# Performance work log

Hardware: AMD Instinct MI355X
Metric: run time of the kernel (lower is better)

Reference implementation:

```python
import jax, jax.numpy as jnp
import numpy as np

NUM_HEADS = 12
TOP_K = 4
LN_EPS = 1e-5


def _ln(x, w, b):
    m = jnp.mean(x, -1, keepdims=True)
    v = jnp.mean((x - m) ** 2, -1, keepdims=True)
    return (x - m) * jax.lax.rsqrt(v + LN_EPS) * w + b


def _attn(x, qkv_w, qkv_b, proj_w, proj_b):
    B, N, C = x.shape
    hd = C // NUM_HEADS
    qkv = (x @ qkv_w + qkv_b).reshape(B, N, 3, NUM_HEADS, hd)
    q, k, v = jnp.moveaxis(qkv, 2, 0)  # each [B,N,H,hd]
    attn = jax.nn.softmax(jnp.einsum('bnhd,bmhd->bhnm', q * hd ** -0.5, k), axis=-1)
    out = jnp.einsum('bhnm,bmhd->bnhd', attn, v).reshape(B, N, C)
    return out @ proj_w + proj_b


def _moe(x2, gate_w, w1, b1, w2, b2):
    # x2: [tokens, D]; vmoe-style token top-k gating (eval mode, no noise)
    Tt = x2.shape[0]
    E = gate_w.shape[1]
    probs = jax.nn.softmax(x2 @ gate_w, axis=-1)            # [tokens, E]
    topv, topi = jax.lax.top_k(probs, TOP_K)                # [tokens, K]
    combine = jnp.zeros((Tt, E), x2.dtype).at[jnp.arange(Tt)[:, None], topi].set(topv)
    h = jax.nn.gelu(jnp.einsum('td,edh->teh', x2, w1) + b1[None], approximate=False)
    y = jnp.einsum('teh,ehd->ted', h, w2) + b2[None]
    return jnp.einsum('ted,te->td', y, combine)


def reference(x, ln1a_w, ln1a_b, qkv_wa, qkv_ba, proj_wa, proj_ba, ln2a_w, ln2a_b,
              fc1_w, fc1_b, fc2_w, fc2_b,
              ln1b_w, ln1b_b, qkv_wb, qkv_bb, proj_wb, proj_bb, ln2b_w, ln2b_b,
              gate_w, w1, b1, w2, b2, head_w, head_b,
              shared_masks, agg_mask):
    B, N, D = x.shape
    # dense ViT block
    x = x + _attn(_ln(x, ln1a_w, ln1a_b), qkv_wa, qkv_ba, proj_wa, proj_ba)
    h = _ln(x, ln2a_w, ln2a_b)
    x = x + (jax.nn.gelu(h @ fc1_w + fc1_b, approximate=False) @ fc2_w + fc2_b)
    # MoE ViT block
    x = x + _attn(_ln(x, ln1b_w, ln1b_b), qkv_wb, qkv_bb, proj_wb, proj_bb)
    h = _ln(x, ln2b_w, ln2b_b).reshape(B * N, D)
    x = x + _moe(h, gate_w, w1, b1, w2, b2).reshape(B, N, D)
    # per-task heads + masked multi-task aggregation (Aggregation.forward)
    task_out = jnp.einsum('bnd,tdo->tbno', x, head_w) + head_b[:, None, None, :]
    valid = (shared_masks & agg_mask[None]).astype(x.dtype)[..., None]  # [T,B,N,1]
    summed = (task_out * valid).sum(0)
    count = valid.sum(0)
    return summed / (count + 1e-6)


def setup_inputs() -> dict:
    key = jax.random.key(0)
    ks = jax.random.split(key, 32)
    B, N, D, HID, E, T = 8, 197, 768, 3072, 8, 8
    f = lambda k, shape: (jax.random.normal(k, shape, jnp.float32) * 0.02)
    return {
        'x': jax.random.normal(ks[0], (B, N, D), jnp.float32),
        'ln1a_w': jnp.ones((D,)), 'ln1a_b': jnp.zeros((D,)),
        'qkv_wa': f(ks[1], (D, 3 * D)), 'qkv_ba': jnp.zeros((3 * D,)),
        'proj_wa': f(ks[2], (D, D)), 'proj_ba': jnp.zeros((D,)),
        'ln2a_w': jnp.ones((D,)), 'ln2a_b': jnp.zeros((D,)),
        'fc1_w': f(ks[3], (D, HID)), 'fc1_b': jnp.zeros((HID,)),
        'fc2_w': f(ks[4], (HID, D)), 'fc2_b': jnp.zeros((D,)),
        'ln1b_w': jnp.ones((D,)), 'ln1b_b': jnp.zeros((D,)),
        'qkv_wb': f(ks[5], (D, 3 * D)), 'qkv_bb': jnp.zeros((3 * D,)),
        'proj_wb': f(ks[6], (D, D)), 'proj_bb': jnp.zeros((D,)),
        'ln2b_w': jnp.ones((D,)), 'ln2b_b': jnp.zeros((D,)),
        'gate_w': f(ks[7], (D, E)),
        'w1': f(ks[8], (E, D, HID)), 'b1': jnp.zeros((E, HID)),
        'w2': f(ks[9], (E, HID, D)), 'b2': jnp.zeros((E, D)),
        'head_w': f(ks[10], (T, D, D)), 'head_b': jnp.zeros((T, D)),
        'shared_masks': jax.random.bernoulli(ks[11], 0.5, (T, B, N)),
        'agg_mask': jax.random.bernoulli(ks[12], 0.5, (B, N)),
    }
```

## Files before the change

### kernel.cpp

```cpp
#include <hip/hip_runtime.h>
#include <hip/hip_bf16.h>

#define DEV static __device__ __forceinline__

typedef short bfx8 __attribute__((ext_vector_type(8)));
typedef float fx4  __attribute__((ext_vector_type(4)));

DEV float bf2f(__hip_bfloat16 h) { return __bfloat162float(h); }
DEV __hip_bfloat16 f2bf(float f) { return __float2bfloat16(f); }
DEV float uLO(unsigned u) { return __uint_as_float(u << 16); }
DEV unsigned short f2bfu(float f) { __hip_bfloat16 h = __float2bfloat16(f); return *(unsigned short*)&h; }

DEV float wave_sum(float v) {
#pragma unroll
  for (int o = 32; o; o >>= 1) v += __shfl_xor(v, o, 64);
  return v;
}

#define GLD_LDS16(gp, lp) __builtin_amdgcn_global_load_lds( \
    (__attribute__((address_space(1))) void*)(gp),          \
    (__attribute__((address_space(3))) void*)(lp), 16, 0, 0)

struct TDesc { const float* src; __hip_bfloat16* dst; int R, C, nz, tilesPerZ, tileOff; };
struct TPack { TDesc d[9]; int n; };

__global__ __launch_bounds__(256) void transpose_all_k(TPack p) {
  __shared__ unsigned short t[64 * 66];
  const int bid = blockIdx.x;
  int di = 0;
#pragma unroll
  for (int i = 1; i < 9; ++i)
    if (i < p.n && bid >= p.d[i].tileOff) di = i;
  const TDesc d = p.d[di];
  int local = bid - d.tileOff;
  int z = local / d.tilesPerZ;
  int rem = local - z * d.tilesPerZ;
  int ctiles = d.C >> 6;
  int bx = rem % ctiles, by = rem / ctiles;
  const float* src = d.src + (size_t)z * d.R * d.C;
  __hip_bfloat16* dst = d.dst + (size_t)z * d.R * d.C;
  int c0 = bx * 64, r0 = by * 64;
  const int tid = threadIdx.x;
#pragma unroll
  for (int it = 0; it < 4; ++it) {
    int idx = tid + it * 256;
    int row = idx >> 4, q = idx & 15;
    float4 v = *(const float4*)(src + (size_t)(r0 + row) * d.C + c0 + q * 4);
    ushort2 lo, hi;
    lo.x = f2bfu(v.x); lo.y = f2bfu(v.y);
    hi.x = f2bfu(v.z); hi.y = f2bfu(v.w);
    *(ushort2*)&t[row * 66 + q * 4]     = lo;
    *(ushort2*)&t[row * 66 + q * 4 + 2] = hi;
  }
  __syncthreads();
#pragma unroll
  for (int it = 0; it < 2; ++it) {
    int idx = tid + it * 256;
    int oc = idx >> 3, q = idx & 7;
    bfx8 w;
#pragma unroll
    for (int j = 0; j < 8; ++j)
      w[j] = (short)t[(q * 8 + j) * 66 + oc];
    *(bfx8*)(dst + (size_t)(c0 + oc) * d.R + r0 + q * 8) = w;
  }
}

__global__ __launch_bounds__(256) void transpose_k(
    const float* __restrict__ src, __hip_bfloat16* __restrict__ dst,
    int R, int C)
{
  __shared__ float tile[32][33];
  size_t off = (size_t)blockIdx.z * R * C;
  src += off; dst += off;
  int c0 = blockIdx.x * 32, r0 = blockIdx.y * 32;
#pragma unroll
  for (int i = 0; i < 32; i += 8)
    tile[threadIdx.y + i][threadIdx.x] =
        src[(size_t)(r0 + threadIdx.y + i) * C + c0 + threadIdx.x];
  __syncthreads();
#pragma unroll
  for (int i = 0; i < 32; i += 8)
    dst[(size_t)(c0 + threadIdx.y + i) * R + r0 + threadIdx.x] =
        f2bf(tile[threadIdx.x][threadIdx.y + i]);
}

enum { EPI_STORE = 0, EPI_GELU = 1, EPI_RESADD = 2, EPI_MOE = 3,
       EPI_GELU_R = 4, EPI_MOEP = 5, EPI_HEAD_R = 6, EPI_HEADP = 7 };

template <int MODE>
__global__ __launch_bounds__(256) void gemm_bt(
    const __hip_bfloat16* __restrict__ A,
    const __hip_bfloat16* __restrict__ BT,
    const float* __restrict__ bias,
    int M, int N, int K, int splitK, int taskBase,
    long long strideBz, long long strideBiasz, long long strideAz, long long strideCz,
    __hip_bfloat16* __restrict__ Cb, float* __restrict__ Cf,
    const float* __restrict__ combine, const int* __restrict__ rt)
{
  constexpr bool ROUTED = (MODE == EPI_GELU_R || MODE == EPI_MOEP ||
                           MODE == EPI_HEAD_R || MODE == EPI_HEADP);
  constexpr bool GATHER = (MODE == EPI_GELU_R || MODE == EPI_HEAD_R || MODE == EPI_HEADP);
  __shared__ __hip_bfloat16 sA[2][128 * 32];
  __shared__ __hip_bfloat16 sB[2][128 * 32];
  const int tid = threadIdx.x;
  const int wave = tid >> 6, lane = tid & 63;
  const int quad = lane >> 4, l16 = lane & 15;
  const int z = blockIdx.z;
  const int zt = z / splitK;
  const int kc = z - zt * splitK;
  const int task = taskBase + zt;
  const int Ksub = K / splitK;
  const int kbeg = kc * Ksub;
  const int m0 = blockIdx.y * 128, n0 = blockIdx.x * 128;

  int Meff = M;
  int rtb = 0;
  const int* ilist = nullptr;
  if (ROUTED) {
    const int base = (MODE == EPI_HEAD_R || MODE == EPI_HEADP) ? 8 : 0;
    Meff = rt[base + zt];
    ilist = rt + 32 + (size_t)base * M + (size_t)zt * M;
    if (MODE == EPI_MOEP) rtb = rt[16 + zt];
    if (MODE == EPI_HEADP) rtb = rt[24 + zt];
    if (m0 >= Meff) return;
  }

  A += (size_t)zt * strideAz;
  if (MODE != EPI_MOEP && MODE != EPI_HEADP) Cb += (size_t)zt * strideCz;
  const __hip_bfloat16* Bz = BT + (size_t)zt * strideBz;
  const float* biasz = bias + (size_t)zt * strideBiasz;
  const int wm = (wave >> 1) * 64, wn = (wave & 1) * 64;

  fx4 acc[4][4];
#pragma unroll
  for (int i = 0; i < 4; ++i)
#pragma unroll
    for (int j = 0; j < 4; ++j) acc[i][j] = (fx4){0.f, 0.f, 0.f, 0.f};

  const int c0 = tid, c1 = tid + 256;
  const int mlim = Meff - 1;
  int gm0 = m0 + (c0 >> 2); if (gm0 > mlim) gm0 = mlim;
  int gm1 = m0 + (c1 >> 2); if (gm1 > mlim) gm1 = mlim;
  const int ar0 = GATHER ? ilist[gm0] : gm0;
  const int ar1 = GATHER ? ilist[gm1] : gm1;
  const int ak0 = (c0 & 3) * 8, ak1 = (c1 & 3) * 8;
  const __hip_bfloat16* pa0 = A + (size_t)ar0 * K + kbeg + ak0;
  const __hip_bfloat16* pa1 = A + (size_t)ar1 * K + kbeg + ak1;
  const __hip_bfloat16* pb0 = Bz + (size_t)(n0 + (c0 >> 2)) * K + kbeg + ak0;
  const __hip_bfloat16* pb1 = Bz + (size_t)(n0 + (c1 >> 2)) * K + kbeg + ak1;

  GLD_LDS16(pa0, &sA[0][c0 * 8]);
  GLD_LDS16(pa1, &sA[0][c1 * 8]);
  GLD_LDS16(pb0, &sB[0][c0 * 8]);
  GLD_LDS16(pb1, &sB[0][c1 * 8]);
  __syncthreads();

  int cur = 0;
  for (int kk = 0; kk < Ksub; kk += 32) {
    const int nxt = kk + 32;
    if (nxt < Ksub) {
      GLD_LDS16(pa0 + nxt, &sA[cur ^ 1][c0 * 8]);
      GLD_LDS16(pa1 + nxt, &sA[cur ^ 1][c1 * 8]);
      GLD_LDS16(pb0 + nxt, &sB[cur ^ 1][c0 * 8]);
      GLD_LDS16(pb1 + nxt, &sB[cur ^ 1][c1 * 8]);
    }
    bfx8 af[4], bfr[4];
#pragma unroll
    for (int i = 0; i < 4; ++i)
      af[i] = *(const bfx8*)(&sA[cur][(wm + i * 16 + l16) * 32 + quad * 8]);
#pragma unroll
    for (int j = 0; j < 4; ++j)
      bfr[j] = *(const bfx8*)(&sB[cur][(wn + j * 16 + l16) * 32 + quad * 8]);
#pragma unroll
    for (int i = 0; i < 4; ++i)
#pragma unroll
      for (int j = 0; j < 4; ++j)
        acc[i][j] = __builtin_amdgcn_mfma_f32_16x16x32_bf16(af[i], bfr[j], acc[i][j], 0, 0, 0);
    __syncthreads();
    cur ^= 1;
  }

  const int mb = m0 + wm + quad * 4;
  const int nb = n0 + wn + l16;
#pragma unroll
  for (int i = 0; i < 4; ++i) {
#pragma unroll
    for (int rr = 0; rr < 4; ++rr) {
      const int m = mb + i * 16 + rr;
      if (m >= Meff) continue;
      int orow = m;
      if (MODE == EPI_HEAD_R) orow = ilist[m];
#pragma unroll
      for (int j = 0; j < 4; ++j) {
        const int n = nb + j * 16;
        float v = acc[i][j][rr];
        if (MODE == EPI_STORE) {
          Cb[(size_t)m * N + n] = f2bf(v + biasz[n]);
        } else if (MODE == EPI_GELU || MODE == EPI_GELU_R) {
          float t = v + biasz[n];
          Cb[(size_t)m * N + n] = f2bf(0.5f * t * (1.f + erff(t * 0.70710678118654752f)));
        } else if (MODE == EPI_RESADD) {
          if (kc == 0) v += biasz[n];
          atomicAdd(&Cf[(size_t)m * N + n], v);
        } else if (MODE == EPI_MOE) {
          float s = combine[m * 8 + task];
          if (s != 0.f) {
            if (kc == 0) v += biasz[n];
            atomicAdd(&Cf[(size_t)m * N + n], s * v);
          }
        } else if (MODE == EPI_MOEP) {
          if (kc == 0) v += biasz[n];
          Cf[(size_t)kc * strideCz + (size_t)(rtb + m) * N + n] = v;
        } else if (MODE == EPI_HEADP) {
          Cf[(size_t)(rtb + m) * N + n] = v + biasz[n];
        } else {
          atomicAdd(&Cf[(size_t)orow * N + n], v + biasz[n]);
        }
      }
    }
  }
}

__global__ __launch_bounds__(256) void attn_mfma_k(
    const __hip_bfloat16* __restrict__ qkvb, __hip_bfloat16* __restrict__ outb)
{
  __shared__ __align__(16) unsigned short VT[64 * 232];
  __shared__ __align__(16) unsigned short Pst[4][16 * 232];
  const int tid = threadIdx.x;
  const int chunk = blockIdx.x & 3;
  const int bh = blockIdx.x >> 2;
  const int b = bh / 12, h = bh - b * 12;
  const size_t tokBase = (size_t)b * 197;
  const __hip_bfloat16* qkvh = qkvb + tokBase * 2304 + (size_t)h * 64;

  for (int idx = tid; idx < 197 * 32; idx += 256) {
    int j = idx >> 5, dp = idx & 31;
    unsigned pv = *(const unsigned*)(qkvh + (size_t)j * 2304 + 1536 + dp * 2);
    VT[(2 * dp) * 232 + j]     = (unsigned short)(pv & 0xffffu);
    VT[(2 * dp + 1) * 232 + j] = (unsigned short)(pv >> 16);
  }
  for (int idx = tid; idx < 64 * 35; idx += 256) {
    int r = idx / 35, c = 197 + idx % 35;
    VT[r * 232 + c] = 0;
  }
  __syncthreads();

  const int wave = tid >> 6, lane = tid & 63;
  const int quad = lane >> 4, l16 = lane & 15;
  const int mt = chunk * 4 + wave;
  if (mt >= 13) return;

  {
    int r = lane >> 2, c = 208 + (lane & 3) * 4;
    *(uint2*)&Pst[wave][r * 232 + c] = (uint2){0u, 0u};
  }

  int tq = mt * 16 + l16; if (tq > 196) tq = 196;
  const bfx8 af0 = *(const bfx8*)(qkvh + (size_t)tq * 2304 + quad * 8);
  const bfx8 af1 = *(const bfx8*)(qkvh + (size_t)tq * 2304 + 32 + quad * 8);

  fx4 sv[13];
#pragma unroll
  for (int n0 = 0; n0 < 13; ++n0) {
    int tk = n0 * 16 + l16; if (tk > 196) tk = 196;
    const __hip_bfloat16* kp = qkvh + (size_t)tk * 2304 + 768;
    bfx8 bf0 = *(const bfx8*)(kp + quad * 8);
    bfx8 bf1 = *(const bfx8*)(kp + 32 + quad * 8);
    fx4 a = (fx4){0.f, 0.f, 0.f, 0.f};
    a = __builtin_amdgcn_mfma_f32_16x16x32_bf16(af0, bf0, a, 0, 0, 0);
    a = __builtin_amdgcn_mfma_f32_16x16x32_bf16(af1, bf1, a, 0, 0, 0);
    sv[n0] = a;
  }

  float inv[4];
#pragma unroll
  for (int rr = 0; rr < 4; ++rr) {
    float mx = -3.0e38f;
#pragma unroll
    for (int n0 = 0; n0 < 13; ++n0) {
      bool ok = (n0 < 12) | (l16 < 5);
      float s = ok ? sv[n0][rr] * 0.125f : -3.0e38f;
      sv[n0][rr] = s;
      mx = fmaxf(mx, s);
    }
#pragma unroll
    for (int o = 1; o < 16; o <<= 1) mx = fmaxf(mx, __shfl_xor(mx, o, 64));
    float sum = 0.f;
#pragma unroll
    for (int n0 = 0; n0 < 13; ++n0) {
      float s = sv[n0][rr];
      float e = (s > -1.0e38f) ? __expf(s - mx) : 0.f;
      sv[n0][rr] = e;
      sum += e;
    }
#pragma unroll
    for (int o = 1; o < 16; o <<= 1) sum += __shfl_xor(sum, o, 64);
    inv[rr] = 1.f / sum;
    const int row = quad * 4 + rr;
#pragma unroll
    for (int n0 = 0; n0 < 13; ++n0)
      Pst[wave][row * 232 + n0 * 16 + l16] = f2bfu(sv[n0][rr]);
  }

  fx4 pv[4];
#pragma unroll
  for (int nd = 0; nd < 4; ++nd) pv[nd] = (fx4){0.f, 0.f, 0.f, 0.f};
#pragma unroll
  for (int kk = 0; kk < 7; ++kk) {
    bfx8 paf = *(const bfx8*)&Pst[wave][l16 * 232 + kk * 32 + quad * 8];
#pragma unroll
    for (int nd = 0; nd < 4; ++nd) {
      bfx8 bfv = *(const bfx8*)&VT[(nd * 16 + l16) * 232 + kk * 32 + quad * 8];
      pv[nd] = __builtin_amdgcn_mfma_f32_16x16x32_bf16(paf, bfv, pv[nd], 0, 0, 0);
    }
  }

#pragma unroll
  for (int rr = 0; rr < 4; ++rr) {
    const int row = quad * 4 + rr;
#pragma unroll
    for (int n0 = 0; n0 < 13; ++n0) {
      float e = sv[n0][rr];
      Pst[wave][row * 232 + n0 * 16 + l16] = f2bfu(e - uLO(f2bfu(e)));
    }
  }

#pragma unroll
  for (int kk = 0; kk < 7; ++kk) {
    bfx8 paf = *(const bfx8*)&Pst[wave][l16 * 232 + kk * 32 + quad * 8];
#pragma unroll
    for (int nd = 0; nd < 4; ++nd) {
      bfx8 bfv = *(const bfx8*)&VT[(nd * 16 + l16) * 232 + kk * 32 + quad * 8];
      pv[nd] = __builtin_amdgcn_mfma_f32_16x16x32_bf16(paf, bfv, pv[nd], 0, 0, 0);
    }
  }

#pragma unroll
  for (int rr = 0; rr < 4; ++rr) {
    int m = mt * 16 + quad * 4 + rr;
    if (m > 196) continue;
    __hip_bfloat16* op = outb + (tokBase + m) * 768 + (size_t)h * 64;
#pragma unroll
    for (int nd = 0; nd < 4; ++nd)
      op[nd * 16 + l16] = f2bf(pv[nd][rr] * inv[rr]);
  }
}

__global__ __launch_bounds__(256) void ln_k(
    const float* __restrict__ xf, const float* __restrict__ w,
    const float* __restrict__ b, __hip_bfloat16* __restrict__ out, int T)
{
  int wv = threadIdx.x >> 6, lane = threadIdx.x & 63;
  int t = blockIdx.x * 4 + wv;
  if (t >= T) return;
  const float* row = xf + (size_t)t * 768;
  float v[12]; float s = 0.f;
#pragma unroll
  for (int i = 0; i < 12; ++i) { v[i] = row[lane + i * 64]; s += v[i]; }
  s = wave_sum(s);
  float mean = s * (1.f / 768.f);
  float q = 0.f;
#pragma unroll
  for (int i = 0; i < 12; ++i) { float d = v[i] - mean; q += d * d; }
  q = wave_sum(q);
  float rstd = rsqrtf(q * (1.f / 768.f) + 1e-5f);
#pragma unroll
  for (int i = 0; i < 12; ++i) {
    int d = lane + i * 64;
    out[(size_t)t * 768 + d] = f2bf((v[i] - mean) * rstd * w[d] + b[d]);
  }
}

__global__ __launch_bounds__(256) void gate_k(
    const float* __restrict__ xf, const float* __restrict__ lw,
    const float* __restrict__ lb, const float* __restrict__ gw,
    float* __restrict__ combine, int* __restrict__ rt, int* __restrict__ smap,
    __hip_bfloat16* __restrict__ lnbout, int T)
{
  int wv = threadIdx.x >> 6, lane = threadIdx.x & 63;
  int t = blockIdx.x * 4 + wv;
  if (t >= T) return;
  const float* row = xf + (size_t)t * 768;
  float v[12]; float s = 0.f;
#pragma unroll
  for (int i = 0; i < 12; ++i) { v[i] = row[lane + i * 64]; s += v[i]; }
  s = wave_sum(s);
  float mean = s * (1.f / 768.f);
  float qv = 0.f;
#pragma unroll
  for (int i = 0; i < 12; ++i) { float d = v[i] - mean; qv += d * d; }
  qv = wave_sum(qv);
  float rstd = rsqrtf(qv * (1.f / 768.f) + 1e-5f);
  float acc[8];
#pragma unroll
  for (int e = 0; e < 8; ++e) acc[e] = 0.f;
#pragma unroll
  for (int i = 0; i < 12; ++i) {
    int d = lane + i * 64;
    float xn = (v[i] - mean) * rstd * lw[d] + lb[d];
    lnbout[(size_t)t * 768 + d] = f2bf(xn);
    float4 g0 = *(const float4*)(gw + (size_t)d * 8);
    float4 g1 = *(const float4*)(gw + (size_t)d * 8 + 4);
    acc[0] += xn * g0.x; acc[1] += xn * g0.y;
    acc[2] += xn * g0.z; acc[3] += xn * g0.w;
    acc[4] += xn * g1.x; acc[5] += xn * g1.y;
    acc[6] += xn * g1.z; acc[7] += xn * g1.w;
  }
#pragma unroll
  for (int e = 0; e < 8; ++e) acc[e] = wave_sum(acc[e]);
  float mx = acc[0];
#pragma unroll
  for (int e = 1; e < 8; ++e) mx = fmaxf(mx, acc[e]);
  float p[8]; float se = 0.f;
#pragma unroll
  for (int e = 0; e < 8; ++e) { p[e] = __expf(acc[e] - mx); se += p[e]; }
  float inv = 1.f / se;
#pragma unroll
  for (int e = 0; e < 8; ++e) p[e] *= inv;
  float outv[8]; bool used[8];
#pragma unroll
  for (int e = 0; e < 8; ++e) { outv[e] = 0.f; used[e] = false; }
  for (int k = 0; k < 4; ++k) {
    int best = -1; float bv = -1.f;
#pragma unroll
    for (int e = 0; e < 8; ++e) if (!used[e] && p[e] > bv) { bv = p[e]; best = e; }
#pragma unroll
    for (int e = 0; e < 8; ++e) if (e == best) { used[e] = true; outv[e] = bv; }
  }
#pragma unroll
  for (int e = 0; e < 8; ++e) if (lane == e) combine[(size_t)t * 8 + e] = outv[e];
#pragma unroll
  for (int e = 0; e < 8; ++e)
    if (lane == e && outv[e] != 0.f) {
      int slot = atomicAdd(&rt[e], 1);
      rt[32 + e * T + slot] = t;
      smap[(size_t)t * 8 + e] = slot;
    }
}

__global__ void prefix_k(int* __restrict__ rt) {
  if (threadIdx.x == 0) {
    int s = 0;
#pragma unroll
    for (int e = 0; e < 8; ++e) { rt[16 + e] = s; s += rt[e]; }
    int s2 = 0;
#pragma unroll
    for (int tt = 0; tt < 8; ++tt) { rt[24 + tt] = s2; s2 += rt[8 + tt]; }
  }
}

__global__ __launch_bounds__(256) void combine_k(
    const float* __restrict__ y, const float* __restrict__ combine,
    const int* __restrict__ rt, const int* __restrict__ smap,
    float* __restrict__ xf, __hip_bfloat16* __restrict__ lnbout, int T, int CAP)
{
  int wv = threadIdx.x >> 6, lane = threadIdx.x & 63;
  int t = blockIdx.x * 4 + wv;
  if (t >= T) return;
  float acc[12];
#pragma unroll
  for (int i = 0; i < 12; ++i) acc[i] = 0.f;
  for (int e = 0; e < 8; ++e) {
    float s = combine[(size_t)t * 8 + e];
    if (s != 0.f) {
      int r = rt[16 + e] + smap[(size_t)t * 8 + e];
      const float* y0 = y + (size_t)r * 768;
      const float* y1 = y0 + (size_t)CAP * 768;
#pragma unroll
      for (int i = 0; i < 12; ++i)
        acc[i] += s * (y0[lane + i * 64] + y1[lane + i * 64]);
    }
  }
  float* xr = xf + (size_t)t * 768;
#pragma unroll
  for (int i = 0; i < 12; ++i) {
    float nv = xr[lane + i * 64] + acc[i];
    xr[lane + i * 64] = nv;
    lnbout[(size_t)t * 768 + lane + i * 64] = f2bf(nv);
  }
}

__global__ void mask_k(const int* __restrict__ sm, const int* __restrict__ am,
                       float* __restrict__ cnt, int* __restrict__ rt,
                       int* __restrict__ tsmap, int* __restrict__ valid, int T)
{
  int t = blockIdx.x * 256 + threadIdx.x;
  if (t >= T) return;
  int a = am[t] != 0;
  float c = 0.f;
#pragma unroll
  for (int tt = 0; tt < 8; ++tt) {
    int vv = (sm[tt * T + t] != 0) & a;
    valid[tt * T + t] = vv;
    int slot = -1;
    if (vv) {
      slot = atomicAdd(&rt[8 + tt], 1);
      rt[32 + 8 * T + tt * T + slot] = t;
    }
    tsmap[(size_t)t * 8 + tt] = slot;
    c += (float)vv;
  }
  cnt[t] = c;
}

__global__ void f2b_k(const float* __restrict__ in, __hip_bfloat16* __restrict__ out, int n) {
  int i = blockIdx.x * 256 + threadIdx.x;
  if (i < n) out[i] = f2bf(in[i]);
}
__global__ void final_k(float* __restrict__ out, const float* __restrict__ cnt, int n) {
  int i = blockIdx.x * 256 + threadIdx.x;
  if (i < n) out[i] = out[i] / (cnt[i / 768] + 1e-6f);
}
__global__ __launch_bounds__(256) void final2_k(
    const float* __restrict__ y2, const int* __restrict__ rt,
    const int* __restrict__ tsmap, const float* __restrict__ cnt,
    float* __restrict__ out, int T)
{
  int wv = threadIdx.x >> 6, lane = threadIdx.x & 63;
  int t = blockIdx.x * 4 + wv;
  if (t >= T) return;
  float acc[12];
#pragma unroll
  for (int i = 0; i < 12; ++i) acc[i] = 0.f;
  for (int tt = 0; tt < 8; ++tt) {
    int s = tsmap[(size_t)t * 8 + tt];
    if (s >= 0) {
      const float* yr = y2 + (size_t)(rt[24 + tt] + s) * 768;
#pragma unroll
      for (int i = 0; i < 12; ++i) acc[i] += yr[lane + i * 64];
    }
  }
  float inv = 1.f / (cnt[t] + 1e-6f);
  float* orow = out + (size_t)t * 768;
#pragma unroll
  for (int i = 0; i < 12; ++i) orow[lane + i * 64] = acc[i] * inv;
}

extern "C" void kernel_launch(void* const* d_in, const int* in_sizes, int n_in,
                              void* d_out, int out_size, void* d_ws, size_t ws_size,
                              hipStream_t stream)
{
  (void)in_sizes; (void)n_in; (void)out_size;
  const int Ttok = 8 * 197;
  const int D = 768, HID = 3072;
  const int CAP = 4 * Ttok;

  const float* x       = (const float*)d_in[0];
  const float* ln1a_w  = (const float*)d_in[1];
  const float* ln1a_b  = (const float*)d_in[2];
  const float* qkv_wa  = (const float*)d_in[3];
  const float* qkv_ba  = (const float*)d_in[4];
  const float* proj_wa = (const float*)d_in[5];
  const float* proj_ba = (const float*)d_in[6];
  const float* ln2a_w  = (const float*)d_in[7];
  const float* ln2a_b  = (const float*)d_in[8];
  const float* fc1_w   = (const float*)d_in[9];
  const float* fc1_b   = (const float*)d_in[10];
  const float* fc2_w   = (const float*)d_in[11];
  const float* fc2_b   = (const float*)d_in[12];
  const float* ln1b_w  = (const float*)d_in[13];
  const float* ln1b_b  = (const float*)d_in[14];
  const float* qkv_wb  = (const float*)d_in[15];
  const float* qkv_bb  = (const float*)d_in[16];
  const float* proj_wb = (const float*)d_in[17];
  const float* proj_bb = (const float*)d_in[18];
  const float* ln2b_w  = (const float*)d_in[19];
  const float* ln2b_b  = (const float*)d_in[20];
  const float* gate_w  = (const float*)d_in[21];
  const float* w1      = (const float*)d_in[22];
  const float* b1      = (const float*)d_in[23];
  const float* w2      = (const float*)d_in[24];
  const float* b2      = (const float*)d_in[25];
  const float* head_w  = (const float*)d_in[26];
  const float* head_b  = (const float*)d_in[27];
  const int* shared_masks = (const int*)d_in[28];
  const int* agg_mask     = (const int*)d_in[29];
  float* out           = (float*)d_out;

  char* wsp = (char*)d_ws;
  auto alloc = [&](size_t bytes) { char* p = wsp; wsp += (bytes + 255) & ~(size_t)255; return p; };
  float* xf             = (float*)alloc((size_t)Ttok * D * 4);
  __hip_bfloat16* lnb   = (__hip_bfloat16*)alloc((size_t)Ttok * D * 2);
  __hip_bfloat16* qkvb  = (__hip_bfloat16*)alloc((size_t)Ttok * 3 * D * 2);
  __hip_bfloat16* attnb = (__hip_bfloat16*)alloc((size_t)Ttok * D * 2);
  __hip_bfloat16* h1    = (__hip_bfloat16*)alloc((size_t)Ttok * HID * 2);
  float* combine        = (float*)alloc((size_t)Ttok * 8 * 4);
  float* cnt            = (float*)alloc((size_t)Ttok * 4);
  int* rt               = (int*)alloc((size_t)(32 + 16 * Ttok) * 4);
  int* smap             = (int*)alloc((size_t)Ttok * 8 * 4);
  int* tsmap            = (int*)alloc((size_t)Ttok * 8 * 4);
  int* valid            = (int*)alloc((size_t)8 * Ttok * 4);
  __hip_bfloat16* qkvaT = (__hip_bfloat16*)alloc((size_t)D * 3 * D * 2);
  __hip_bfloat16* projaT= (__hip_bfloat16*)alloc((size_t)D * D * 2);
  __hip_bfloat16* fc1T  = (__hip_bfloat16*)alloc((size_t)D * HID * 2);
  __hip_bfloat16* fc2T  = (__hip_bfloat16*)alloc((size_t)D * HID * 2);
  __hip_bfloat16* qkvbT = (__hip_bfloat16*)alloc((size_t)D * 3 * D * 2);
  __hip_bfloat16* projbT= (__hip_bfloat16*)alloc((size_t)D * D * 2);
  __hip_bfloat16* headT = (__hip_bfloat16*)alloc((size_t)8 * D * D * 2);
  __hip_bfloat16* wT    = (__hip_bfloat16*)alloc((size_t)D * HID * 2);

  const size_t used = (size_t)(wsp - (char*)d_ws);
  const size_t extraNeed = 2 * ((size_t)8 * D * HID * 2 + 255)
                         + ((size_t)8 * Ttok * HID * 2 + 255)
                         + (2 * (size_t)CAP * D * 4 + 255);
  const bool batched = (ws_size >= used + extraNeed);
  __hip_bfloat16* w1T8 = nullptr; __hip_bfloat16* w2T8 = nullptr; __hip_bfloat16* h1_8 = nullptr;
  float* yb = nullptr;
  if (batched) {
    w1T8 = (__hip_bfloat16*)alloc((size_t)8 * D * HID * 2);
    w2T8 = (__hip_bfloat16*)alloc((size_t)8 * D * HID * 2);
    h1_8 = (__hip_bfloat16*)alloc((size_t)8 * Ttok * HID * 2);
    yb   = (float*)alloc(2 * (size_t)CAP * D * 4);
  }

  dim3 tb(32, 8);
  if (batched) {
    TPack p; int off = 0;
    auto addT = [&](int i, const float* s, __hip_bfloat16* dd, int R, int C, int nz) {
      int tpz = (R / 64) * (C / 64);
      p.d[i] = TDesc{s, dd, R, C, nz, tpz, off};
      off += tpz * nz;
    };
    addT(0, qkv_wa, qkvaT, D, 3 * D, 1);
    addT(1, proj_wa, projaT, D, D, 1);
    addT(2, fc1_w, fc1T, D, HID, 1);
    addT(3, fc2_w, fc2T, HID, D, 1);
    addT(4, qkv_wb, qkvbT, D, 3 * D, 1);
    addT(5, proj_wb, projbT, D, D, 1);
    addT(6, head_w, headT, D, D, 8);
    addT(7, w1, w1T8, D, HID, 8);
    addT(8, w2, w2T8, HID, D, 8);
    p.n = 9;
    transpose_all_k<<<off, 256, 0, stream>>>(p);
  } else {
    transpose_k<<<dim3(3*D/32, D/32, 1), tb, 0, stream>>>(qkv_wa, qkvaT, D, 3*D);
    transpose_k<<<dim3(D/32, D/32, 1),   tb, 0, stream>>>(proj_wa, projaT, D, D);
    transpose_k<<<dim3(HID/32, D/32, 1), tb, 0, stream>>>(fc1_w, fc1T, D, HID);
    transpose_k<<<dim3(D/32, HID/32, 1), tb, 0, stream>>>(fc2_w, fc2T, HID, D);
    transpose_k<<<dim3(3*D/32, D/32, 1), tb, 0, stream>>>(qkv_wb, qkvbT, D, 3*D);
    transpose_k<<<dim3(D/32, D/32, 1),   tb, 0, stream>>>(proj_wb, projbT, D, D);
    transpose_k<<<dim3(D/32, D/32, 8),   tb, 0, stream>>>(head_w, headT, D, D);
  }

  const int nTok = Ttok * D;
  hipMemcpyAsync(xf, x, (size_t)nTok * 4, hipMemcpyDeviceToDevice, stream);
  hipMemsetAsync(rt, 0, 128, stream);
  mask_k<<<(Ttok + 255)/256, 256, 0, stream>>>(shared_masks, agg_mask, cnt, rt, tsmap, valid, Ttok);
  if (!batched) hipMemsetAsync(out, 0, (size_t)nTok * 4, stream);

  const int lnGrid = (Ttok + 3) / 4;
  dim3 g_qkv(3*D/128, 13, 1);
  dim3 g_proj(D/128, 13, 4);
  dim3 g_fc1(HID/128, 13, 1);
  dim3 g_fc2(D/128, 13, 4);
  dim3 g_head(D/128, 13, 8);
  const int attnGrid = 96 * 4;

  ln_k<<<lnGrid, 256, 0, stream>>>(xf, ln1a_w, ln1a_b, lnb, Ttok);
  gemm_bt<EPI_STORE><<<g_qkv, 256, 0, stream>>>(lnb, qkvaT, qkv_ba, Ttok, 3*D, D, 1, 0, 0, 0, 0, 0, qkvb, nullptr, nullptr, nullptr);
  attn_mfma_k<<<attnGrid, 256, 0, stream>>>(qkvb, attnb);
  gemm_bt<EPI_RESADD><<<g_proj, 256, 0, stream>>>(attnb, projaT, proj_ba, Ttok, D, D, 4, 0, 0, 0, 0, 0, nullptr, xf, nullptr, nullptr);
  ln_k<<<lnGrid, 256, 0, stream>>>(xf, ln2a_w, ln2a_b, lnb, Ttok);
  gemm_bt<EPI_GELU><<<g_fc1, 256, 0, stream>>>(lnb, fc1T, fc1_b, Ttok, HID, D, 1, 0, 0, 0, 0, 0, h1, nullptr, nullptr, nullptr);
  gemm_bt<EPI_RESADD><<<g_fc2, 256, 0, stream>>>(h1, fc2T, fc2_b, Ttok, D, HID, 4, 0, 0, 0, 0, 0, nullptr, xf, nullptr, nullptr);

  ln_k<<<lnGrid, 256, 0, stream>>>(xf, ln1b_w, ln1b_b, lnb, Ttok);
  gemm_bt<EPI_STORE><<<g_qkv, 256, 0, stream>>>(lnb, qkvbT, qkv_bb, Ttok, 3*D, D, 1, 0, 0, 0, 0, 0, qkvb, nullptr, nullptr, nullptr);
  attn_mfma_k<<<attnGrid, 256, 0, stream>>>(qkvb, attnb);
  gemm_bt<EPI_RESADD><<<g_proj, 256, 0, stream>>>(attnb, projbT, proj_bb, Ttok, D, D, 4, 0, 0, 0, 0, 0, nullptr, xf, nullptr, nullptr);
  gate_k<<<lnGrid, 256, 0, stream>>>(xf, ln2b_w, ln2b_b, gate_w, combine, rt, smap, lnb, Ttok);
  prefix_k<<<1, 64, 0, stream>>>(rt);
  if (batched) {
    gemm_bt<EPI_GELU_R><<<dim3(HID/128, 13, 8), 256, 0, stream>>>(
        lnb, w1T8, b1, Ttok, HID, D, 1, 0,
        (long long)D*HID, HID, 0, (long long)Ttok*HID, h1_8, nullptr, nullptr, rt);
    gemm_bt<EPI_MOEP><<<dim3(D/128, 13, 16), 256, 0, stream>>>(
        h1_8, w2T8, b2, Ttok, D, HID, 2, 0,
        (long long)HID*D, D, (long long)Ttok*HID, (long long)CAP*D, nullptr, yb, nullptr, rt);
    combine_k<<<lnGrid, 256, 0, stream>>>(yb, combine, rt, smap, xf, lnb, Ttok, CAP);
    gemm_bt<EPI_HEADP><<<g_head, 256, 0, stream>>>(lnb, headT, head_b, Ttok, D, D, 1, 0, (long long)D*D, D, 0, 0, nullptr, yb, nullptr, rt);
    final2_k<<<lnGrid, 256, 0, stream>>>(yb, rt, tsmap, cnt, out, Ttok);
  } else {
    for (int e = 0; e < 8; ++e) {
      transpose_k<<<dim3(HID/32, D/32, 1), tb, 0, stream>>>(w1 + (size_t)e*D*HID, wT, D, HID);
      gemm_bt<EPI_GELU><<<g_fc1, 256, 0, stream>>>(lnb, wT, b1 + (size_t)e*HID, Ttok, HID, D, 1, 0, 0, 0, 0, 0, h1, nullptr, nullptr, nullptr);
      transpose_k<<<dim3(D/32, HID/32, 1), tb, 0, stream>>>(w2 + (size_t)e*HID*D, wT, HID, D);
      gemm_bt<EPI_MOE><<<g_fc2, 256, 0, stream>>>(h1, wT, b2 + (size_t)e*D, Ttok, D, HID, 4, e, 0, 0, 0, 0, nullptr, xf, combine, nullptr);
    }
    f2b_k<<<(nTok + 255)/256, 256, 0, stream>>>(xf, lnb, nTok);
    gemm_bt<EPI_HEAD_R><<<g_head, 256, 0, stream>>>(lnb, headT, head_b, Ttok, D, D, 1, 0, (long long)D*D, D, 0, 0, nullptr, out, nullptr, rt);
    final_k<<<(nTok + 255)/256, 256, 0, stream>>>(out, cnt, nTok);
  }
}
```

Measured before the change: 816.1 us.

## Interleave weight transpose tiles into earlier GEMM launches as extra blocks

The single upfront transpose of all weights is split up. Only the first QKV weight is transposed before the pipeline starts. Each later weight's transpose tiles are added as extra z-slices to an earlier GEMM launch, so they run alongside that GEMM's blocks, each one a launch ahead of the GEMM that consumes it. This is meant to hide the weight conversion cost behind compute that already has spare CUs. In exchange the GEMM kernel gains a TPack argument, a branch, and a unified shared-memory buffer, which may slightly raise register or argument overhead.

```diff
diff --git a/kernel.cpp b/kernel.cpp
--- a/kernel.cpp
+++ b/kernel.cpp
@@ -24,15 +24,13 @@
 struct TDesc { const float* src; __hip_bfloat16* dst; int R, C, nz, tilesPerZ, tileOff; };
 struct TPack { TDesc d[9]; int n; };
 
-__global__ __launch_bounds__(256) void transpose_all_k(TPack p) {
-  __shared__ unsigned short t[64 * 66];
-  const int bid = blockIdx.x;
+DEV void trans_tile(const TPack& p, int gtile, unsigned short* t, int tid) {
   int di = 0;
 #pragma unroll
   for (int i = 1; i < 9; ++i)
-    if (i < p.n && bid >= p.d[i].tileOff) di = i;
+    if (i < p.n && gtile >= p.d[i].tileOff) di = i;
   const TDesc d = p.d[di];
-  int local = bid - d.tileOff;
+  int local = gtile - d.tileOff;
   int z = local / d.tilesPerZ;
   int rem = local - z * d.tilesPerZ;
   int ctiles = d.C >> 6;
@@ -40,7 +38,6 @@
   const float* src = d.src + (size_t)z * d.R * d.C;
   __hip_bfloat16* dst = d.dst + (size_t)z * d.R * d.C;
   int c0 = bx * 64, r0 = by * 64;
-  const int tid = threadIdx.x;
 #pragma unroll
   for (int it = 0; it < 4; ++it) {
     int idx = tid + it * 256;
@@ -65,6 +62,11 @@
   }
 }
 
+__global__ __launch_bounds__(256) void transpose_all_k(TPack p, int tStart) {
+  __shared__ __align__(16) unsigned short t[64 * 66];
+  trans_tile(p, tStart + blockIdx.x, t, threadIdx.x);
+}
+
 __global__ __launch_bounds__(256) void transpose_k(
     const float* __restrict__ src, __hip_bfloat16* __restrict__ dst,
     int R, int C)
@@ -95,14 +97,22 @@
     int M, int N, int K, int splitK, int taskBase,
     long long strideBz, long long strideBiasz, long long strideAz, long long strideCz,
     __hip_bfloat16* __restrict__ Cb, float* __restrict__ Cf,
-    const float* __restrict__ combine, const int* __restrict__ rt)
+    const float* __restrict__ combine, const int* __restrict__ rt,
+    TPack tp, int tZBase, int tStart, int tCount)
 {
   constexpr bool ROUTED = (MODE == EPI_GELU_R || MODE == EPI_MOEP ||
                            MODE == EPI_HEAD_R || MODE == EPI_HEADP);
   constexpr bool GATHER = (MODE == EPI_GELU_R || MODE == EPI_HEAD_R || MODE == EPI_HEADP);
-  __shared__ __hip_bfloat16 sA[2][128 * 32];
-  __shared__ __hip_bfloat16 sB[2][128 * 32];
+  __shared__ __align__(16) __hip_bfloat16 smem[4 * 128 * 32];
   const int tid = threadIdx.x;
+
+  if ((int)blockIdx.z >= tZBase) {
+    int flat = ((int)blockIdx.z - tZBase) * (int)(gridDim.x * gridDim.y)
+             + (int)blockIdx.y * (int)gridDim.x + (int)blockIdx.x;
+    if (flat < tCount) trans_tile(tp, tStart + flat, (unsigned short*)smem, tid);
+    return;
+  }
+
   const int wave = tid >> 6, lane = tid & 63;
   const int quad = lane >> 4, l16 = lane & 15;
   const int z = blockIdx.z;
@@ -130,6 +140,11 @@
   const __hip_bfloat16* Bz = BT + (size_t)zt * strideBz;
   const float* biasz = bias + (size_t)zt * strideBiasz;
   const int wm = (wave >> 1) * 64, wn = (wave & 1) * 64;
+
+  __hip_bfloat16* sA0 = smem;
+  __hip_bfloat16* sA1 = smem + 128 * 32;
+  __hip_bfloat16* sB0 = smem + 2 * 128 * 32;
+  __hip_bfloat16* sB1 = smem + 3 * 128 * 32;
 
   fx4 acc[4][4];
 #pragma unroll
@@ -149,28 +164,30 @@
   const __hip_bfloat16* pb0 = Bz + (size_t)(n0 + (c0 >> 2)) * K + kbeg + ak0;
   const __hip_bfloat16* pb1 = Bz + (size_t)(n0 + (c1 >> 2)) * K + kbeg + ak1;
 
-  GLD_LDS16(pa0, &sA[0][c0 * 8]);
-  GLD_LDS16(pa1, &sA[0][c1 * 8]);
-  GLD_LDS16(pb0, &sB[0][c0 * 8]);
-  GLD_LDS16(pb1, &sB[0][c1 * 8]);
+  GLD_LDS16(pa0, &sA0[c0 * 8]);
+  GLD_LDS16(pa1, &sA0[c1 * 8]);
+  GLD_LDS16(pb0, &sB0[c0 * 8]);
+  GLD_LDS16(pb1, &sB0[c1 * 8]);
   __syncthreads();
 
   int cur = 0;
   for (int kk = 0; kk < Ksub; kk += 32) {
     const int nxt = kk + 32;
     if (nxt < Ksub) {
-      GLD_LDS16(pa0 + nxt, &sA[cur ^ 1][c0 * 8]);
-      GLD_LDS16(pa1 + nxt, &sA[cur ^ 1][c1 * 8]);
-      GLD_LDS16(pb0 + nxt, &sB[cur ^ 1][c0 * 8]);
-      GLD_LDS16(pb1 + nxt, &sB[cur ^ 1][c1 * 8]);
-    }
+      GLD_LDS16(pa0 + nxt, (cur ? &sA0[c0 * 8] : &sA1[c0 * 8]));
+      GLD_LDS16(pa1 + nxt, (cur ? &sA0[c1 * 8] : &sA1[c1 * 8]));
+      GLD_LDS16(pb0 + nxt, (cur ? &sB0[c0 * 8] : &sB1[c0 * 8]));
+      GLD_LDS16(pb1 + nxt, (cur ? &sB0[c1 * 8] : &sB1[c1 * 8]));
+    }
+    const __hip_bfloat16* sAc = cur ? sA1 : sA0;
+    const __hip_bfloat16* sBc = cur ? sB1 : sB0;
     bfx8 af[4], bfr[4];
 #pragma unroll
     for (int i = 0; i < 4; ++i)
-      af[i] = *(const bfx8*)(&sA[cur][(wm + i * 16 + l16) * 32 + quad * 8]);
+      af[i] = *(const bfx8*)(&sAc[(wm + i * 16 + l16) * 32 + quad * 8]);
 #pragma unroll
     for (int j = 0; j < 4; ++j)
-      bfr[j] = *(const bfx8*)(&sB[cur][(wn + j * 16 + l16) * 32 + quad * 8]);
+      bfr[j] = *(const bfx8*)(&sBc[(wn + j * 16 + l16) * 32 + quad * 8]);
 #pragma unroll
     for (int i = 0; i < 4; ++i)
 #pragma unroll
@@ -614,24 +631,26 @@
   }
 
   dim3 tb(32, 8);
+  TPack pk{}; pk.n = 0;
+  int o_proj_wa = 0, o_fc2 = 0, o_proj_wb = 0, o_w1 = 0, o_w2 = 0, oTot = 0;
   if (batched) {
-    TPack p; int off = 0;
+    int off = 0;
     auto addT = [&](int i, const float* s, __hip_bfloat16* dd, int R, int C, int nz) {
       int tpz = (R / 64) * (C / 64);
-      p.d[i] = TDesc{s, dd, R, C, nz, tpz, off};
+      pk.d[i] = TDesc{s, dd, R, C, nz, tpz, off};
       off += tpz * nz;
     };
-    addT(0, qkv_wa, qkvaT, D, 3 * D, 1);
+    addT(0, qkv_wa, qkvaT, D, 3 * D, 1);   o_proj_wa = off;
     addT(1, proj_wa, projaT, D, D, 1);
-    addT(2, fc1_w, fc1T, D, HID, 1);
+    addT(2, fc1_w, fc1T, D, HID, 1);       o_fc2 = pk.d[2].tileOff + (D/64)*(HID/64);
     addT(3, fc2_w, fc2T, HID, D, 1);
-    addT(4, qkv_wb, qkvbT, D, 3 * D, 1);
+    addT(4, qkv_wb, qkvbT, D, 3 * D, 1);   o_proj_wb = pk.d[4].tileOff + (D/64)*(3*D/64);
     addT(5, proj_wb, projbT, D, D, 1);
-    addT(6, head_w, headT, D, D, 8);
-    addT(7, w1, w1T8, D, HID, 8);
+    addT(6, head_w, headT, D, D, 8);       o_w1 = pk.d[6].tileOff + 8*(D/64)*(D/64);
+    addT(7, w1, w1T8, D, HID, 8);          o_w2 = pk.d[7].tileOff + 8*(D/64)*(HID/64);
     addT(8, w2, w2T8, HID, D, 8);
-    p.n = 9;
-    transpose_all_k<<<off, 256, 0, stream>>>(p);
+    pk.n = 9; oTot = off;
+    transpose_all_k<<<o_proj_wa, 256, 0, stream>>>(pk, 0);
   } else {
     transpose_k<<<dim3(3*D/32, D/32, 1), tb, 0, stream>>>(qkv_wa, qkvaT, D, 3*D);
     transpose_k<<<dim3(D/32, D/32, 1),   tb, 0, stream>>>(proj_wa, projaT, D, D);
@@ -649,6 +668,10 @@
   if (!batched) hipMemsetAsync(out, 0, (size_t)nTok * 4, stream);
 
   const int lnGrid = (Ttok + 3) / 4;
+  auto carry = [&](dim3 g, int cnt) {
+    if (cnt > 0) { int ps = g.x * g.y; g.z += (cnt + ps - 1) / ps; }
+    return g;
+  };
   dim3 g_qkv(3*D/128, 13, 1);
   dim3 g_proj(D/128, 13, 4);
   dim3 g_fc1(HID/128, 13, 1);
@@ -656,39 +679,50 @@
   dim3 g_head(D/128, 13, 8);
   const int attnGrid = 96 * 4;
 
+  int w1half = batched ? (o_w2 - o_w1) / 2 : 0;
+  int w2half = batched ? (oTot - o_w2) / 2 : 0;
+  int s1 = o_proj_wa, c1 = o_fc2 - o_proj_wa;
+  int s2 = o_fc2,     c2 = o_proj_wb - o_fc2;
+  int s3 = o_proj_wb, c3 = o_w1 - o_proj_wb;
+  int s4 = o_w1,      c4 = w1half;
+  int s5 = o_w1 + w1half, c5 = (o_w2 - o_w1) - w1half;
+  int s6 = o_w2,      c6 = w2half;
+  int s7 = o_w2 + w2half, c7 = (oTot - o_w2) - w2half;
+  if (!batched) { c1 = c2 = c3 = c4 = c5 = c6 = c7 = 0; }
+
   ln_k<<<lnGrid, 256, 0, stream>>>(xf, ln1a_w, ln1a_b, lnb, Ttok);
-  gemm_bt<EPI_STORE><<<g_qkv, 256, 0, stream>>>(lnb, qkvaT, qkv_ba, Ttok, 3*D, D, 1, 0, 0, 0, 0, 0, qkvb, nullptr, nullptr, nullptr);
+  gemm_bt<EPI_STORE><<<carry(g_qkv, c1), 256, 0, stream>>>(lnb, qkvaT, qkv_ba, Ttok, 3*D, D, 1, 0, 0, 0, 0, 0, qkvb, nullptr, nullptr, nullptr, pk, 1, s1, c1);
   attn_mfma_k<<<attnGrid, 256, 0, stream>>>(qkvb, attnb);
-  gemm_bt<EPI_RESADD><<<g_proj, 256, 0, stream>>>(attnb, projaT, proj_ba, Ttok, D, D, 4, 0, 0, 0, 0, 0, nullptr, xf, nullptr, nullptr);
+  gemm_bt<EPI_RESADD><<<carry(g_proj, c2), 256, 0, stream>>>(attnb, projaT, proj_ba, Ttok, D, D, 4, 0, 0, 0, 0, 0, nullptr, xf, nullptr, nullptr, pk, 4, s2, c2);
   ln_k<<<lnGrid, 256, 0, stream>>>(xf, ln2a_w, ln2a_b, lnb, Ttok);
-  gemm_bt<EPI_GELU><<<g_fc1, 256, 0, stream>>>(lnb, fc1T, fc1_b, Ttok, HID, D, 1, 0, 0, 0, 0, 0, h1, nullptr, nullptr, nullptr);
-  gemm_bt<EPI_RESADD><<<g_fc2, 256, 0, stream>>>(h1, fc2T, fc2_b, Ttok, D, HID, 4, 0, 0, 0, 0, 0, nullptr, xf, nullptr, nullptr);
+  gemm_bt<EPI_GELU><<<carry(g_fc1, c3), 256, 0, stream>>>(lnb, fc1T, fc1_b, Ttok, HID, D, 1, 0, 0, 0, 0, 0, h1, nullptr, nullptr, nullptr, pk, 1, s3, c3);
+  gemm_bt<EPI_RESADD><<<carry(g_fc2, c4), 256, 0, stream>>>(h1, fc2T, fc2_b, Ttok, D, HID, 4, 0, 0, 0, 0, 0, nullptr, xf, nullptr, nullptr, pk, 4, s4, c4);
 
   ln_k<<<lnGrid, 256, 0, stream>>>(xf, ln1b_w, ln1b_b, lnb, Ttok);
-  gemm_bt<EPI_STORE><<<g_qkv, 256, 0, stream>>>(lnb, qkvbT, qkv_bb, Ttok, 3*D, D, 1, 0, 0, 0, 0, 0, qkvb, nullptr, nullptr, nullptr);
+  gemm_bt<EPI_STORE><<<carry(g_qkv, c5), 256, 0, stream>>>(lnb, qkvbT, qkv_bb, Ttok, 3*D, D, 1, 0, 0, 0, 0, 0, qkvb, nullptr, nullptr, nullptr, pk, 1, s5, c5);
   attn_mfma_k<<<attnGrid, 256, 0, stream>>>(qkvb, attnb);
-  gemm_bt<EPI_RESADD><<<g_proj, 256, 0, stream>>>(attnb, projbT, proj_bb, Ttok, D, D, 4, 0, 0, 0, 0, 0, nullptr, xf, nullptr, nullptr);
+  gemm_bt<EPI_RESADD><<<carry(g_proj, c6), 256, 0, stream>>>(attnb, projbT, proj_bb, Ttok, D, D, 4, 0, 0, 0, 0, 0, nullptr, xf, nullptr, nullptr, pk, 4, s6, c6);
   gate_k<<<lnGrid, 256, 0, stream>>>(xf, ln2b_w, ln2b_b, gate_w, combine, rt, smap, lnb, Ttok);
   prefix_k<<<1, 64, 0, stream>>>(rt);
   if (batched) {
-    gemm_bt<EPI_GELU_R><<<dim3(HID/128, 13, 8), 256, 0, stream>>>(
+    gemm_bt<EPI_GELU_R><<<carry(dim3(HID/128, 13, 8), c7), 256, 0, stream>>>(
         lnb, w1T8, b1, Ttok, HID, D, 1, 0,
-        (long long)D*HID, HID, 0, (long long)Ttok*HID, h1_8, nullptr, nullptr, rt);
+        (long long)D*HID, HID, 0, (long long)Ttok*HID, h1_8, nullptr, nullptr, rt, pk, 8, s7, c7);
     gemm_bt<EPI_MOEP><<<dim3(D/128, 13, 16), 256, 0, stream>>>(
         h1_8, w2T8, b2, Ttok, D, HID, 2, 0,
-        (long long)HID*D, D, (long long)Ttok*HID, (long long)CAP*D, nullptr, yb, nullptr, rt);
+        (long long)HID*D, D, (long long)Ttok*HID, (long long)CAP*D, nullptr, yb, nullptr, rt, pk, 16, 0, 0);
     combine_k<<<lnGrid, 256, 0, stream>>>(yb, combine, rt, smap, xf, lnb, Ttok, CAP);
-    gemm_bt<EPI_HEADP><<<g_head, 256, 0, stream>>>(lnb, headT, head_b, Ttok, D, D, 1, 0, (long long)D*D, D, 0, 0, nullptr, yb, nullptr, rt);
+    gemm_bt<EPI_HEADP><<<g_head, 256, 0, stream>>>(lnb, headT, head_b, Ttok, D, D, 1, 0, (long long)D*D, D, 0, 0, nullptr, yb, nullptr, rt, pk, 8, 0, 0);
     final2_k<<<lnGrid, 256, 0, stream>>>(yb, rt, tsmap, cnt, out, Ttok);
   } else {
     for (int e = 0; e < 8; ++e) {
       transpose_k<<<dim3(HID/32, D/32, 1), tb, 0, stream>>>(w1 + (size_t)e*D*HID, wT, D, HID);
-      gemm_bt<EPI_GELU><<<g_fc1, 256, 0, stream>>>(lnb, wT, b1 + (size_t)e*HID, Ttok, HID, D, 1, 0, 0, 0, 0, 0, h1, nullptr, nullptr, nullptr);
+      gemm_bt<EPI_GELU><<<g_fc1, 256, 0, stream>>>(lnb, wT, b1 + (size_t)e*HID, Ttok, HID, D, 1, 0, 0, 0, 0, 0, h1, nullptr, nullptr, nullptr, pk, 1, 0, 0);
       transpose_k<<<dim3(D/32, HID/32, 1), tb, 0, stream>>>(w2 + (size_t)e*HID*D, wT, HID, D);
-      gemm_bt<EPI_MOE><<<g_fc2, 256, 0, stream>>>(h1, wT, b2 + (size_t)e*D, Ttok, D, HID, 4, e, 0, 0, 0, 0, nullptr, xf, combine, nullptr);
+      gemm_bt<EPI_MOE><<<g_fc2, 256, 0, stream>>>(h1, wT, b2 + (size_t)e*D, Ttok, D, HID, 4, e, 0, 0, 0, 0, nullptr, xf, combine, nullptr, pk, 4, 0, 0);
     }
     f2b_k<<<(nTok + 255)/256, 256, 0, stream>>>(xf, lnb, nTok);
-    gemm_bt<EPI_HEAD_R><<<g_head, 256, 0, stream>>>(lnb, headT, head_b, Ttok, D, D, 1, 0, (long long)D*D, D, 0, 0, nullptr, out, nullptr, rt);
+    gemm_bt<EPI_HEAD_R><<<g_head, 256, 0, stream>>>(lnb, headT, head_b, Ttok, D, D, 1, 0, (long long)D*D, D, 0, 0, nullptr, out, nullptr, rt, pk, 8, 0, 0);
     final_k<<<(nTok + 255)/256, 256, 0, stream>>>(out, cnt, nTok);
   }
 }
```

Result: faster. 746.5 us (-8.5%).
